# Kernel optimization log

Hardware: AMD Instinct MI355X
Metric: run time of the kernel (lower is better)

The kernel has to match this reference:

```python
import jax, jax.numpy as jnp
import numpy as np

N, E, B, DIM, NF, EF, HID = 50000, 100000, 2000, 64, 14, 4, 128


def setup_inputs() -> dict:
    key = jax.random.key(0)
    ks = jax.random.split(key, 30)
    rn = lambda k, shape, scale: jax.random.normal(k, shape, jnp.float32) * scale
    inp = {}
    inp["x"] = rn(ks[0], (N, NF), 1.0)
    inp["edge_attr"] = jax.random.uniform(ks[1], (E, EF), jnp.float32)
    inp["edge_index"] = jax.random.randint(ks[2], (2, E), 0, N)
    # equal-size graphs: 25 nodes per graph, sorted segment ids
    inp["batch"] = (jnp.arange(N, dtype=jnp.int32) // (N // B)).astype(jnp.int32)
    inp["lin0_w"] = rn(ks[3], (DIM, NF), (1.0 / NF) ** 0.5)
    inp["lin0_b"] = jnp.zeros((DIM,), jnp.float32)
    inp["mlp_w1"] = rn(ks[4], (HID, EF), (1.0 / EF) ** 0.5)
    inp["mlp_b1"] = jnp.zeros((HID,), jnp.float32)
    inp["mlp_w2"] = rn(ks[5], (DIM * DIM, HID), (1.0 / HID) ** 0.5)
    inp["mlp_b2"] = jnp.zeros((DIM * DIM,), jnp.float32)
    inp["root"] = rn(ks[6], (DIM, DIM), (1.0 / DIM) ** 0.5)
    inp["conv_b"] = jnp.zeros((DIM,), jnp.float32)
    inp["gru_wih"] = rn(ks[7], (3 * DIM, DIM), (1.0 / DIM) ** 0.5)
    inp["gru_whh"] = rn(ks[8], (3 * DIM, DIM), (1.0 / DIM) ** 0.5)
    inp["gru_bih"] = jnp.zeros((3 * DIM,), jnp.float32)
    inp["gru_bhh"] = jnp.zeros((3 * DIM,), jnp.float32)
    inp["lstm_wih"] = rn(ks[9], (4 * DIM, 2 * DIM), (1.0 / (2 * DIM)) ** 0.5)
    inp["lstm_whh"] = rn(ks[10], (4 * DIM, DIM), (1.0 / DIM) ** 0.5)
    inp["lstm_bih"] = jnp.zeros((4 * DIM,), jnp.float32)
    inp["lstm_bhh"] = jnp.zeros((4 * DIM,), jnp.float32)
    inp["lin1_w"] = rn(ks[11], (DIM, 2 * DIM), (1.0 / (2 * DIM)) ** 0.5)
    inp["lin1_b"] = jnp.zeros((DIM,), jnp.float32)
    inp["lin2_w"] = rn(ks[12], (1, DIM), (1.0 / DIM) ** 0.5)
    inp["lin2_b"] = jnp.zeros((1,), jnp.float32)
    return inp


def _forward(x, edge_attr, edge_index, batch, lin0_w, lin0_b, mlp_w1, mlp_b1,
             mlp_w2, mlp_b2, root, conv_b, gru_wih, gru_whh, gru_bih, gru_bhh,
             lstm_wih, lstm_whh, lstm_bih, lstm_bhh, lin1_w, lin1_b, lin2_w, lin2_b):
    src, dst = edge_index[0], edge_index[1]
    n = x.shape[0]
    # edge MLP -> per-edge weight matrices [E, DIM, DIM]
    h_e = jax.nn.relu(edge_attr @ mlp_w1.T + mlp_b1)
    W_e = (h_e @ mlp_w2.T + mlp_b2).reshape(-1, DIM, DIM)
    deg = jnp.clip(jax.ops.segment_sum(jnp.ones_like(dst, jnp.float32), dst, n), 1.0)

    out = jax.nn.relu(x @ lin0_w.T + lin0_b)
    h = out  # GRU hidden (seq_len=1, 1 layer)
    for _ in range(3):
        msg = jnp.einsum('ei,eio->eo', out[src], W_e)  # per-edge matmul
        agg = jax.ops.segment_sum(msg, dst, n) / deg[:, None]  # scatter-mean
        m = jax.nn.relu(agg + out @ root + conv_b)  # NNConv: aggr + root + bias
        # GRU step
        gi = m @ gru_wih.T + gru_bih
        gh = h @ gru_whh.T + gru_bhh
        i_r, i_z, i_n = jnp.split(gi, 3, axis=-1)
        h_r, h_z, h_n = jnp.split(gh, 3, axis=-1)
        r = jax.nn.sigmoid(i_r + h_r)
        z = jax.nn.sigmoid(i_z + h_z)
        ng = jnp.tanh(i_n + r * h_n)
        h = (1.0 - z) * ng + z * h
        out = h

    # Set2Set pooling, 3 processing steps
    b = B
    qh = jnp.zeros((b, DIM), out.dtype)
    qc = jnp.zeros((b, DIM), out.dtype)
    q_star = jnp.zeros((b, 2 * DIM), out.dtype)
    for _ in range(3):
        gates = q_star @ lstm_wih.T + lstm_bih + qh @ lstm_whh.T + lstm_bhh
        gi_, gf_, gg_, go_ = jnp.split(gates, 4, axis=-1)
        qc = jax.nn.sigmoid(gf_) * qc + jax.nn.sigmoid(gi_) * jnp.tanh(gg_)
        qh = jax.nn.sigmoid(go_) * jnp.tanh(qc)
        q = qh
        e = jnp.sum(out * q[batch], axis=-1)  # [N]
        e_max = jax.ops.segment_max(e, batch, b)
        a = jnp.exp(e - e_max[batch])
        denom = jax.ops.segment_sum(a, batch, b)
        a = a / denom[batch]
        r_read = jax.ops.segment_sum(a[:, None] * out, batch, b)
        q_star = jnp.concatenate([q, r_read], axis=-1)

    y = jax.nn.relu(q_star @ lin1_w.T + lin1_b)
    y = y @ lin2_w.T + lin2_b
    return y.reshape(-1)


def reference(x, edge_attr, edge_index, batch, lin0_w, lin0_b, mlp_w1, mlp_b1,
              mlp_w2, mlp_b2, root, conv_b, gru_wih, gru_whh, gru_bih, gru_bhh,
              lstm_wih, lstm_whh, lstm_bih, lstm_bhh, lin1_w, lin1_b, lin2_w, lin2_b):
    return _forward(x, edge_attr, edge_index, batch, lin0_w, lin0_b, mlp_w1, mlp_b1,
                    mlp_w2, mlp_b2, root, conv_b, gru_wih, gru_whh, gru_bih, gru_bhh,
                    lstm_wih, lstm_whh, lstm_bih, lstm_bhh, lin1_w, lin1_b, lin2_w, lin2_b)
```

## Files before the change

kernel.cpp:

```cpp
#include <hip/hip_runtime.h>
#include <hip/hip_bf16.h>

#define NN 50000
#define EE 100000
#define BB 2000
#define DIM 64
#define NF 14
#define EF 4
#define HID 128
#define EPAD 100096
#define EPAD2 100352

typedef __attribute__((ext_vector_type(8))) _Float16 half8;
typedef __attribute__((ext_vector_type(4))) _Float16 half4;
typedef __attribute__((ext_vector_type(4))) float floatx4;

__device__ __forceinline__ float rcp_fast(float x) { return __builtin_amdgcn_rcpf(x); }
__device__ __forceinline__ float sig_fast(float x) { return rcp_fast(1.f + __expf(-x)); }
__device__ __forceinline__ float tanh_fast(float x) {
    float e = __expf(2.f * x);
    return 1.f - 2.f * rcp_fast(e + 1.f);
}

__global__ void prep_fused_kernel(
    const float* __restrict__ x, const float* __restrict__ lin0_w,
    const float* __restrict__ lin0_b, float* __restrict__ hv,
    const float* __restrict__ ea, const float* __restrict__ w1,
    const float* __restrict__ b1, _Float16* __restrict__ he,
    const int* __restrict__ ei, float* __restrict__ deg,
    const float* __restrict__ w2, _Float16* __restrict__ W2rT,
    const float* __restrict__ lih, const float* __restrict__ lhh,
    const float* __restrict__ l1, float* __restrict__ lihT,
    float* __restrict__ lhhT, float* __restrict__ l1T,
    const float* __restrict__ root, const float* __restrict__ b2,
    const float* __restrict__ gwih, const float* __restrict__ gwhh,
    const float* __restrict__ gbih, const float* __restrict__ gbhh,
    _Float16* __restrict__ W1h, _Float16* __restrict__ W2h,
    float* __restrict__ fbias) {
    int t = blockIdx.x * 256 + threadIdx.x;

    {
        int el = t >> 4, hc = t & 15;
        if (el < EPAD2) {
            half8 o8 = {0, 0, 0, 0, 0, 0, 0, 0};
            if (el < EE) {
                const float4 a = *(const float4*)(ea + (size_t)el * 4);
                #pragma unroll
                for (int j = 0; j < 8; j++) {
                    int h = hc * 8 + j;
                    const float4 w = *(const float4*)(w1 + h * 4);
                    float acc = fmaxf(b1[h] + a.x * w.x + a.y * w.y + a.z * w.z + a.w * w.w, 0.f);
                    o8[j] = (_Float16)acc;
                }
                if (hc == 0) atomicAdd(&deg[ei[EE + el]], 1.0f);
            }
            *(half8*)(he + (size_t)el * 128 + hc * 8) = o8;
        }
    }
    if (t < NN * 8) {
        int n = t >> 3, dc = t & 7;
        float xv[NF];
        #pragma unroll
        for (int f = 0; f < NF; f++) xv[f] = x[(size_t)n * NF + f];
        float o[8];
        #pragma unroll
        for (int j = 0; j < 8; j++) {
            int d = dc * 8 + j;
            float acc = lin0_b[d];
            #pragma unroll
            for (int f = 0; f < NF; f++) acc += xv[f] * lin0_w[d * NF + f];
            o[j] = fmaxf(acc, 0.f);
        }
        *(float4*)(hv + (size_t)n * 64 + dc * 8)     = make_float4(o[0], o[1], o[2], o[3]);
        *(float4*)(hv + (size_t)n * 64 + dc * 8 + 4) = make_float4(o[4], o[5], o[6], o[7]);
    }
    if (t < 64 * 1024) {
        int o = t >> 10, kc = t & 1023;
        int k0 = kc * 8, i = k0 >> 7, h0 = k0 & 127;
        const float* src = w2 + (size_t)(i * 64 + o) * 128 + h0;
        const float4 a = *(const float4*)src;
        const float4 b = *(const float4*)(src + 4);
        half8 r = {(_Float16)a.x, (_Float16)a.y, (_Float16)a.z, (_Float16)a.w,
                   (_Float16)b.x, (_Float16)b.y, (_Float16)b.z, (_Float16)b.w};
        *(half8*)(W2rT + (size_t)o * 8192 + k0) = r;
    }
    if (t < 256 * 128) { int j = t / 128, k = t % 128; lihT[k * 256 + j] = lih[t]; }
    if (t < 256 * 64) { int j = t / 64, k = t % 64; lhhT[k * 256 + j] = lhh[t]; }
    if (t < 64 * 128) { int d = t / 128, k = t % 128; l1T[k * 64 + d] = l1[t]; }
    if (t < 64 * 128) {
        int n = t >> 7, k = t & 127;
        W1h[t] = (_Float16)(k < 64 ? root[k * 64 + n] : b2[(size_t)(k - 64) * 64 + n]);
    }
    if (t < 256 * 128) {
        int n2 = t >> 7, k = t & 127;
        int g = n2 >> 6, j = n2 & 63;
        float v;
        if (g == 0)      v = (k < 64) ? gwih[j * 64 + k]         : gwhh[j * 64 + (k - 64)];
        else if (g == 1) v = (k < 64) ? gwih[(64 + j) * 64 + k]  : gwhh[(64 + j) * 64 + (k - 64)];
        else if (g == 2) v = (k < 64) ? gwih[(128 + j) * 64 + k] : 0.f;
        else             v = (k < 64) ? 0.f                      : gwhh[(128 + j) * 64 + (k - 64)];
        W2h[t] = (_Float16)v;
    }
    if (t < 256) {
        int g = t >> 6, j = t & 63;
        float v = (g == 0) ? gbih[j] + gbhh[j]
                : (g == 1) ? gbih[64 + j] + gbhh[64 + j]
                : (g == 2) ? gbih[128 + j] : gbhh[128 + j];
        fbias[t] = v;
    }
}

__global__ __launch_bounds__(256, 2) void msg_gemm_kernel(
    const float* __restrict__ hv, const _Float16* __restrict__ he16,
    const _Float16* __restrict__ W2rT, const int* __restrict__ ei,
    float* __restrict__ agg, float* __restrict__ xsum) {
    __shared__ _Float16 sB[2][16 * 64 * 8];
    __shared__ _Float16 sXs[256 * 68];
    __shared__ int sDst[256];
    const int t = threadIdx.x;
    const int eb = blockIdx.x * 256;
    const int lane = t & 63;
    const int w = t >> 6;
    const int col = lane & 15;
    const int quad = lane >> 4;

    if (t < 256) {
        int e = eb + t;
        sDst[t] = (e < EE) ? ei[EE + e] : 0;
    }
    #pragma unroll 4
    for (int rep = 0; rep < 16; rep++) {
        int idx = rep * 256 + t;
        int el = idx >> 4, d4 = idx & 15;
        int e = eb + el;
        float4 v = {0.f, 0.f, 0.f, 0.f};
        if (e < EE) {
            int src = ei[e];
            v = *(const float4*)(hv + (size_t)src * 64 + d4 * 4);
        }
        half4 h4 = {(_Float16)v.x, (_Float16)v.y, (_Float16)v.z, (_Float16)v.w};
        *(half4*)&sXs[el * 68 + d4 * 4] = h4;
    }

    half8 heReg[4][4];
    #pragma unroll
    for (int mt = 0; mt < 4; mt++) {
        int row = eb + w * 64 + mt * 16 + col;
        #pragma unroll
        for (int p = 0; p < 4; p++)
            heReg[mt][p] = *(const half8*)(he16 + (size_t)row * 128 + p * 32 + quad * 8);
    }

    floatx4 Cacc[4][4];
    #pragma unroll
    for (int mt = 0; mt < 4; mt++)
        #pragma unroll
        for (int nt = 0; nt < 4; nt++)
            Cacc[mt][nt] = (floatx4){0.f, 0.f, 0.f, 0.f};

    const size_t gbase = (size_t)(w * 16 + col) * 8192 + quad * 8;
    half8 pre[4];
    {
        #pragma unroll
        for (int rep = 0; rep < 4; rep++)
            pre[rep] = *(const half8*)(W2rT + gbase + 0 * 128 + rep * 32);
        #pragma unroll
        for (int rep = 0; rep < 4; rep++)
            *(half8*)&sB[0][((w * 4 + rep) * 64 + lane) * 8] = pre[rep];
    }
    __syncthreads();

    #pragma unroll 1
    for (int i = 0; i < 64; i++) {
        int buf = i & 1;
        if (i < 63) {
            #pragma unroll
            for (int rep = 0; rep < 4; rep++)
                pre[rep] = *(const half8*)(W2rT + gbase + (size_t)(i + 1) * 128 + rep * 32);
        }
        _Float16 xsx[4];
        #pragma unroll
        for (int mt = 0; mt < 4; mt++)
            xsx[mt] = sXs[(w * 64 + mt * 16 + col) * 68 + i];
        __builtin_amdgcn_s_setprio(1);
        #pragma unroll
        for (int ks = 0; ks < 4; ks++) {
            half8 bfr[4];
            #pragma unroll
            for (int nt = 0; nt < 4; nt++)
                bfr[nt] = *(const half8*)&sB[buf][((nt * 4 + ks) * 64 + lane) * 8];
            #pragma unroll
            for (int mt = 0; mt < 4; mt++) {
                half8 afr = heReg[mt][ks] * xsx[mt];
                #pragma unroll
                for (int nt = 0; nt < 4; nt++)
                    Cacc[mt][nt] = __builtin_amdgcn_mfma_f32_16x16x32_f16(afr, bfr[nt], Cacc[mt][nt], 0, 0, 0);
            }
        }
        __builtin_amdgcn_s_setprio(0);
        if (i < 63) {
            #pragma unroll
            for (int rep = 0; rep < 4; rep++)
                *(half8*)&sB[buf ^ 1][((w * 4 + rep) * 64 + lane) * 8] = pre[rep];
        }
        __syncthreads();
    }

    #pragma unroll
    for (int mt = 0; mt < 4; mt++) {
        #pragma unroll
        for (int r = 0; r < 4; r++) {
            int el = w * 64 + mt * 16 + quad * 4 + r;
            if (eb + el < EE) {
                float* ap = agg + (size_t)sDst[el] * 64 + col;
                #pragma unroll
                for (int nt = 0; nt < 4; nt++)
                    atomicAdd(ap + nt * 16, Cacc[mt][nt][r]);
            }
        }
    }
    #pragma unroll 4
    for (int rep = 0; rep < 64; rep++) {
        int idx = rep * 256 + t;
        int el = idx >> 6, d = idx & 63;
        if (eb + el < EE)
            atomicAdd(&xsum[(size_t)sDst[el] * 64 + d], (float)sXs[el * 68 + d]);
    }
}

__global__ __launch_bounds__(256, 3) void node_fused_kernel(
    const float* __restrict__ hv_in, float* __restrict__ agg,
    float* __restrict__ xsum, const float* __restrict__ deg,
    const _Float16* __restrict__ W1h, const _Float16* __restrict__ W2h,
    const float* __restrict__ fbias, const float* __restrict__ cb,
    float* __restrict__ hv_out) {
    __shared__ _Float16 sA1[64 * 136];
    __shared__ _Float16 sA2[64 * 136];
    __shared__ float sAgg[64 * 68];
    const int t = threadIdx.x;
    const int nb = blockIdx.x * 64;
    const int n = t >> 2, part = t & 3;
    {
        int gn = nb + n;
        bool valid = gn < NN;
        float inv = 1.f;
        if (valid) inv = 1.f / fmaxf(deg[gn], 1.f);
        #pragma unroll
        for (int c4 = 0; c4 < 4; c4++) {
            int d0 = part * 16 + c4 * 4;
            float4 hvv = {0.f, 0.f, 0.f, 0.f}, agv = {0.f, 0.f, 0.f, 0.f}, xsv = {0.f, 0.f, 0.f, 0.f};
            if (valid) {
                hvv = *(const float4*)(hv_in + (size_t)gn * 64 + d0);
                agv = *(const float4*)(agg + (size_t)gn * 64 + d0);
                xsv = *(const float4*)(xsum + (size_t)gn * 64 + d0);
            }
            agv.x *= inv; agv.y *= inv; agv.z *= inv; agv.w *= inv;
            xsv.x *= inv; xsv.y *= inv; xsv.z *= inv; xsv.w *= inv;
            half4 hvh = {(_Float16)hvv.x, (_Float16)hvv.y, (_Float16)hvv.z, (_Float16)hvv.w};
            half4 xsh = {(_Float16)xsv.x, (_Float16)xsv.y, (_Float16)xsv.z, (_Float16)xsv.w};
            *(half4*)&sA1[n * 136 + d0] = hvh;
            *(half4*)&sA1[n * 136 + 64 + d0] = xsh;
            *(half4*)&sA2[n * 136 + 64 + d0] = hvh;
            *(float4*)&sAgg[n * 68 + d0] = agv;
        }
        if (valid) {
            float4 z = {0.f, 0.f, 0.f, 0.f};
            #pragma unroll
            for (int c4 = 0; c4 < 4; c4++) {
                int d0 = part * 16 + c4 * 4;
                *(float4*)(agg + (size_t)gn * 64 + d0) = z;
                *(float4*)(xsum + (size_t)gn * 64 + d0) = z;
            }
        }
    }
    __syncthreads();

    const int lane = t & 63, w = t >> 6;
    const int col = lane & 15, quad = lane >> 4;

    floatx4 C1[4];
    #pragma unroll
    for (int nt = 0; nt < 4; nt++) {
        float b = cb[nt * 16 + col];
        C1[nt] = (floatx4){b, b, b, b};
    }
    #pragma unroll
    for (int ks = 0; ks < 4; ks++) {
        half8 a = *(const half8*)&sA1[(w * 16 + col) * 136 + ks * 32 + quad * 8];
        #pragma unroll
        for (int nt = 0; nt < 4; nt++) {
            half8 bfr = *(const half8*)(W1h + (size_t)(nt * 16 + col) * 128 + ks * 32 + quad * 8);
            C1[nt] = __builtin_amdgcn_mfma_f32_16x16x32_f16(a, bfr, C1[nt], 0, 0, 0);
        }
    }
    #pragma unroll
    for (int nt = 0; nt < 4; nt++) {
        #pragma unroll
        for (int r = 0; r < 4; r++) {
            int node = w * 16 + quad * 4 + r;
            int j = nt * 16 + col;
            float m = fmaxf(C1[nt][r] + sAgg[node * 68 + j], 0.f);
            sA2[node * 136 + j] = (_Float16)m;
        }
    }
    __syncthreads();

    floatx4 C2[16];
    #pragma unroll
    for (int nt2 = 0; nt2 < 16; nt2++) {
        float b = fbias[nt2 * 16 + col];
        C2[nt2] = (floatx4){b, b, b, b};
    }
    #pragma unroll
    for (int ks = 0; ks < 4; ks++) {
        half8 a = *(const half8*)&sA2[(w * 16 + col) * 136 + ks * 32 + quad * 8];
        #pragma unroll
        for (int nt2 = 0; nt2 < 16; nt2++) {
            half8 bfr = *(const half8*)(W2h + (size_t)(nt2 * 16 + col) * 128 + ks * 32 + quad * 8);
            C2[nt2] = __builtin_amdgcn_mfma_f32_16x16x32_f16(a, bfr, C2[nt2], 0, 0, 0);
        }
    }
    #pragma unroll
    for (int r = 0; r < 4; r++) {
        int node = w * 16 + quad * 4 + r;
        int gn2 = nb + node;
        if (gn2 < NN) {
            #pragma unroll
            for (int jt = 0; jt < 4; jt++) {
                int j = jt * 16 + col;
                float rr = sig_fast(C2[jt][r]);
                float zz = sig_fast(C2[4 + jt][r]);
                float ng = tanh_fast(C2[8 + jt][r] + rr * C2[12 + jt][r]);
                float hold = hv_in[(size_t)gn2 * 64 + j];
                hv_out[(size_t)gn2 * 64 + j] = (1.f - zz) * ng + zz * hold;
            }
        }
    }
}

__global__ __launch_bounds__(256) void set2set_kernel(
    const float* __restrict__ hv,
    const float* __restrict__ lihT, const float* __restrict__ lhhT,
    const float* __restrict__ l_bih, const float* __restrict__ l_bhh,
    const float* __restrict__ lin1T, const float* __restrict__ lin1_b,
    const float* __restrict__ lin2_w, const float* __restrict__ lin2_b,
    float* __restrict__ out) {
    __shared__ float outS[25 * 65];
    __shared__ float qs[128], qh[64], qc[64], gat[256], ew[32], aw[32], red[64];
    int g = blockIdx.x;
    int t = threadIdx.x;
    for (int p = t; p < 25 * 64; p += 256) {
        int j = p >> 6, i = p & 63;
        outS[j * 65 + i] = hv[(size_t)(g * 25 + j) * 64 + i];
    }
    if (t < 128) qs[t] = 0.f;
    if (t < 64) { qh[t] = 0.f; qc[t] = 0.f; }
    __syncthreads();
    for (int it = 0; it < 3; it++) {
        float acc = l_bih[t] + l_bhh[t];
        for (int k = 0; k < 128; k++) acc += qs[k] * lihT[k * 256 + t];
        for (int k = 0; k < 64; k++) acc += qh[k] * lhhT[k * 256 + t];
        gat[t] = acc;
        __syncthreads();
        if (t < 64) {
            float ig = sig_fast(gat[t]);
            float fg = sig_fast(gat[64 + t]);
            float gg = tanh_fast(gat[128 + t]);
            float og = sig_fast(gat[192 + t]);
            float c = fg * qc[t] + ig * gg;
            qc[t] = c;
            qh[t] = og * tanh_fast(c);
        }
        __syncthreads();
        if (t < 25) {
            float e = 0.f;
            for (int i = 0; i < 64; i++) e += outS[t * 65 + i] * qh[i];
            ew[t] = e;
        }
        __syncthreads();
        if (t == 0) {
            float mx = ew[0];
            for (int j = 1; j < 25; j++) mx = fmaxf(mx, ew[j]);
            float s = 0.f;
            for (int j = 0; j < 25; j++) { float a = __expf(ew[j] - mx); aw[j] = a; s += a; }
            float inv = rcp_fast(s);
            for (int j = 0; j < 25; j++) aw[j] *= inv;
        }
        __syncthreads();
        if (t < 64) {
            float r = 0.f;
            for (int j = 0; j < 25; j++) r += aw[j] * outS[j * 65 + t];
            qs[t] = qh[t];
            qs[64 + t] = r;
        }
        __syncthreads();
    }
    if (t < 64) {
        float y1 = lin1_b[t];
        for (int k = 0; k < 128; k++) y1 += qs[k] * lin1T[k * 64 + t];
        y1 = fmaxf(y1, 0.f);
        red[t] = y1 * lin2_w[t];
    }
    __syncthreads();
    if (t == 0) {
        float y = lin2_b[0];
        for (int i = 0; i < 64; i++) y += red[i];
        out[g] = y;
    }
}

extern "C" void kernel_launch(void* const* d_in, const int* in_sizes, int n_in,
                              void* d_out, int out_size, void* d_ws, size_t ws_size,
                              hipStream_t stream) {
    const float* x        = (const float*)d_in[0];
    const float* ea       = (const float*)d_in[1];
    const int*   ei       = (const int*)  d_in[2];
    const float* lin0_w   = (const float*)d_in[4];
    const float* lin0_b   = (const float*)d_in[5];
    const float* mlp_w1   = (const float*)d_in[6];
    const float* mlp_b1   = (const float*)d_in[7];
    const float* mlp_w2   = (const float*)d_in[8];
    const float* mlp_b2   = (const float*)d_in[9];
    const float* root     = (const float*)d_in[10];
    const float* conv_b   = (const float*)d_in[11];
    const float* gru_wih  = (const float*)d_in[12];
    const float* gru_whh  = (const float*)d_in[13];
    const float* gru_bih  = (const float*)d_in[14];
    const float* gru_bhh  = (const float*)d_in[15];
    const float* lstm_wih = (const float*)d_in[16];
    const float* lstm_whh = (const float*)d_in[17];
    const float* lstm_bih = (const float*)d_in[18];
    const float* lstm_bhh = (const float*)d_in[19];
    const float* lin1_w   = (const float*)d_in[20];
    const float* lin1_b   = (const float*)d_in[21];
    const float* lin2_w   = (const float*)d_in[22];
    const float* lin2_b   = (const float*)d_in[23];
    float* out = (float*)d_out;

    char* base = (char*)d_ws;
    size_t off = 0;
    auto carve = [&](size_t bytes) -> void* {
        void* r = base + off;
        off = (off + bytes + 255) & ~(size_t)255;
        return r;
    };
    float* hv   = (float*)carve((size_t)NN * 64 * 4);
    float* agg  = (float*)carve((size_t)NN * 64 * 4);
    float* xsum = (float*)carve((size_t)NN * 64 * 4);
    float* deg  = (float*)carve((size_t)NN * 4);
    float* lihT = (float*)carve(128 * 256 * 4);
    float* lhhT = (float*)carve(64 * 256 * 4);
    float* l1T  = (float*)carve(128 * 64 * 4);
    float* fbias = (float*)carve(256 * 4);
    _Float16* he16 = (_Float16*)carve((size_t)EPAD2 * 128 * 2);
    _Float16* W2rT = (_Float16*)carve((size_t)64 * 8192 * 2);
    _Float16* W1h  = (_Float16*)carve((size_t)64 * 128 * 2);
    _Float16* W2h  = (_Float16*)carve((size_t)256 * 128 * 2);

    hipMemsetAsync(agg, 0, (size_t)NN * 64 * 4 * 2 + (size_t)NN * 4, stream);
    prep_fused_kernel<<<EPAD2 * 16 / 256, 256, 0, stream>>>(
        x, lin0_w, lin0_b, hv,
        ea, mlp_w1, mlp_b1, he16, ei, deg,
        mlp_w2, W2rT,
        lstm_wih, lstm_whh, lin1_w, lihT, lhhT, l1T,
        root, mlp_b2, gru_wih, gru_whh, gru_bih, gru_bhh,
        W1h, W2h, fbias);

    for (int it = 0; it < 3; it++) {
        msg_gemm_kernel<<<EPAD / 256, 256, 0, stream>>>(hv, he16, W2rT, ei, agg, xsum);
        node_fused_kernel<<<(NN + 63) / 64, 256, 0, stream>>>(hv, agg, xsum, deg,
                                                              W1h, W2h, fbias, conv_b, hv);
    }

    set2set_kernel<<<BB, 256, 0, stream>>>(hv, lihT, lhhT, lstm_bih, lstm_bhh,
                                           l1T, lin1_b, lin2_w, lin2_b, out);
}
```

Baseline: 731.9 us.

## Fold agg/xsum zeroing into prep kernel, drop setprio, prefetch GRU hold, warp softmax

Zeroing of the agg and xsum buffers moves from a hipMemsetAsync into the prep kernel, so only deg is still memset separately. The s_setprio hints around the MFMA loop in msg_gemm are removed. The node kernel now loads the previous hidden state before the second GEMM so that load can overlap compute. The set2set softmax switches from a single-thread serial loop to a 32-lane shuffle reduction. Together these trim launch overhead and serial latency, at the cost of more register pressure in the node kernel.

```diff
diff --git a/kernel.cpp b/kernel.cpp
--- a/kernel.cpp
+++ b/kernel.cpp
@@ -36,9 +36,12 @@
     const float* __restrict__ gwih, const float* __restrict__ gwhh,
     const float* __restrict__ gbih, const float* __restrict__ gbhh,
     _Float16* __restrict__ W1h, _Float16* __restrict__ W2h,
-    float* __restrict__ fbias) {
+    float* __restrict__ fbias, float* __restrict__ aggxs) {
     int t = blockIdx.x * 256 + threadIdx.x;
 
+    if (t < NN * 64 * 2 / 4) {
+        ((float4*)aggxs)[t] = make_float4(0.f, 0.f, 0.f, 0.f);
+    }
     {
         int el = t >> 4, hc = t & 15;
         if (el < EPAD2) {
@@ -182,7 +185,6 @@
         #pragma unroll
         for (int mt = 0; mt < 4; mt++)
             xsx[mt] = sXs[(w * 64 + mt * 16 + col) * 68 + i];
-        __builtin_amdgcn_s_setprio(1);
         #pragma unroll
         for (int ks = 0; ks < 4; ks++) {
             half8 bfr[4];
@@ -197,7 +199,6 @@
                     Cacc[mt][nt] = __builtin_amdgcn_mfma_f32_16x16x32_f16(afr, bfr[nt], Cacc[mt][nt], 0, 0, 0);
             }
         }
-        __builtin_amdgcn_s_setprio(0);
         if (i < 63) {
             #pragma unroll
             for (int rep = 0; rep < 4; rep++)
@@ -305,6 +306,16 @@
     }
     __syncthreads();
 
+    float holdv[4][4];
+    #pragma unroll
+    for (int r = 0; r < 4; r++) {
+        int node = w * 16 + quad * 4 + r;
+        int gn2 = nb + node;
+        #pragma unroll
+        for (int jt = 0; jt < 4; jt++)
+            holdv[r][jt] = (gn2 < NN) ? hv_in[(size_t)gn2 * 64 + jt * 16 + col] : 0.f;
+    }
+
     floatx4 C2[16];
     #pragma unroll
     for (int nt2 = 0; nt2 < 16; nt2++) {
@@ -331,8 +342,7 @@
                 float rr = sig_fast(C2[jt][r]);
                 float zz = sig_fast(C2[4 + jt][r]);
                 float ng = tanh_fast(C2[8 + jt][r] + rr * C2[12 + jt][r]);
-                float hold = hv_in[(size_t)gn2 * 64 + j];
-                hv_out[(size_t)gn2 * 64 + j] = (1.f - zz) * ng + zz * hold;
+                hv_out[(size_t)gn2 * 64 + j] = (1.f - zz) * ng + zz * holdv[r][jt];
             }
         }
     }
@@ -378,13 +388,16 @@
             ew[t] = e;
         }
         __syncthreads();
-        if (t == 0) {
-            float mx = ew[0];
-            for (int j = 1; j < 25; j++) mx = fmaxf(mx, ew[j]);
-            float s = 0.f;
-            for (int j = 0; j < 25; j++) { float a = __expf(ew[j] - mx); aw[j] = a; s += a; }
-            float inv = rcp_fast(s);
-            for (int j = 0; j < 25; j++) aw[j] *= inv;
+        if (t < 32) {
+            float e = (t < 25) ? ew[t] : -1e30f;
+            float mx = e;
+            #pragma unroll
+            for (int o = 16; o > 0; o >>= 1) mx = fmaxf(mx, __shfl_xor(mx, o, 32));
+            float a = (t < 25) ? __expf(e - mx) : 0.f;
+            float s = a;
+            #pragma unroll
+            for (int o = 16; o > 0; o >>= 1) s += __shfl_xor(s, o, 32);
+            if (t < 25) aw[t] = a * rcp_fast(s);
         }
         __syncthreads();
         if (t < 64) {
@@ -457,14 +470,14 @@
     _Float16* W1h  = (_Float16*)carve((size_t)64 * 128 * 2);
     _Float16* W2h  = (_Float16*)carve((size_t)256 * 128 * 2);
 
-    hipMemsetAsync(agg, 0, (size_t)NN * 64 * 4 * 2 + (size_t)NN * 4, stream);
+    hipMemsetAsync(deg, 0, (size_t)NN * 4, stream);
     prep_fused_kernel<<<EPAD2 * 16 / 256, 256, 0, stream>>>(
         x, lin0_w, lin0_b, hv,
         ea, mlp_w1, mlp_b1, he16, ei, deg,
         mlp_w2, W2rT,
         lstm_wih, lstm_whh, lin1_w, lihT, lhhT, l1T,
         root, mlp_b2, gru_wih, gru_whh, gru_bih, gru_bhh,
-        W1h, W2h, fbias);
+        W1h, W2h, fbias, agg);
 
     for (int it = 0; it < 3; it++) {
         msg_gemm_kernel<<<EPAD / 256, 256, 0, stream>>>(hv, he16, W2rT, ei, agg, xsum);
```

New measurement: 740.2 us. No clear change (+1.1%).
